# Performance work log

Measured on AMD Instinct MI355X. Metric: run time of the kernel, lower is better.

Reference implementation:

```python
import jax, jax.numpy as jnp
import numpy as np

B, L, INP, HID, NCLS = 512, 256, 300, 256, 5  # trees, leaves/tree, embed dim, hidden, classes


def setup_inputs() -> dict:
    key = jax.random.key(0)
    ks = jax.random.split(key, 7)
    s_in = 1.0 / np.sqrt(INP).astype(np.float32)
    s_h = 1.0 / np.sqrt(HID).astype(np.float32)
    # W_leaf order: [inp_gate, out_gate, upd_gate]
    # W_nl order:  [inp_ln, inp_rn, fo_l_l, fo_l_r, fo_r_l, fo_r_r, out_ln, out_rn, upd_ln, upd_rn]
    return {
        "embeddings": jax.random.normal(ks[0], (B, L, INP), jnp.float32),
        "W_leaf": jax.random.uniform(ks[1], (3, INP, HID), jnp.float32, -s_in, s_in),
        "b_leaf": jax.random.uniform(ks[2], (3, HID), jnp.float32, -s_in, s_in),
        "W_nl": jax.random.uniform(ks[3], (10, HID, HID), jnp.float32, -s_h, s_h),
        "b_nl": jax.random.uniform(ks[4], (10, HID), jnp.float32, -s_h, s_h),
        "W_out": jax.random.uniform(ks[5], (HID, NCLS), jnp.float32, -s_h, s_h),
        "b_out": jax.random.uniform(ks[6], (NCLS,), jnp.float32, -s_h, s_h),
    }


def reference(embeddings, W_leaf, b_leaf, W_nl, b_nl, W_out, b_out):
    sig, tanh = jax.nn.sigmoid, jnp.tanh
    # ---- leaf nodes (depth 0), batched over all B*L leaves ----
    pre = jnp.einsum('bli,gih->blgh', embeddings, W_leaf) + b_leaf  # [B,L,3,H]
    i_g = sig(pre[:, :, 0])
    o_g = sig(pre[:, :, 1])
    u_g = tanh(pre[:, :, 2])
    c = i_g * u_g                      # [B,L,H]
    h = o_g * sig(c)                   # note: leaf uses sigmoid(cell), as in torch code
    logits = [jnp.einsum('bnh,hc->bnc', h, W_out) + b_out]
    # ---- internal nodes, level-synchronous ----
    Wl = W_nl[0::2]                    # [5,H,H] acting on left hidden
    Wr = W_nl[1::2]                    # [5,H,H] acting on right hidden
    bb = b_nl[0::2] + b_nl[1::2]       # [5,H]
    n = L
    while n > 1:
        lc, rc = c[:, 0::2], c[:, 1::2]
        lh, rh = h[:, 0::2], h[:, 1::2]
        pre = (jnp.einsum('bnh,ghk->bngk', lh, Wl)
               + jnp.einsum('bnh,ghk->bngk', rh, Wr) + bb)  # [B,n/2,5,H]
        inp_g = sig(pre[:, :, 0])
        fol_g = sig(pre[:, :, 1])
        for_g = sig(pre[:, :, 2])
        out_g = sig(pre[:, :, 3])
        upd_g = tanh(pre[:, :, 4])
        c = inp_g * upd_g + fol_g * lc + for_g * rc
        h = out_g * tanh(c)
        logits.append(jnp.einsum('bnh,hc->bnc', h, W_out) + b_out)
        n //= 2
    # per-node class scores for all 2L-1 nodes (leaves first, root last)
    return jnp.concatenate(logits, axis=1)  # [B, 2L-1, NCLS]
```

## Files before the change

### kernel.cpp

```cpp
#include <hip/hip_runtime.h>
#include <hip/hip_bf16.h>


#define HID 256

typedef __attribute__((ext_vector_type(8))) short short8;
typedef __attribute__((ext_vector_type(4))) float f32x4;
typedef __attribute__((ext_vector_type(4))) unsigned short ushort4v;

__device__ __forceinline__ float rcpf(float x) { return __builtin_amdgcn_rcpf(x); }
__device__ __forceinline__ float sigf(float x) { return rcpf(1.0f + __expf(-x)); }
__device__ __forceinline__ float tanhf_(float x) { return 2.0f * rcpf(1.0f + __expf(-2.0f * x)) - 1.0f; }
__device__ __forceinline__ float bf2f(unsigned short u) {
    union { unsigned int i; float f; } v; v.i = ((unsigned int)u) << 16; return v.f;
}
__device__ __forceinline__ unsigned short f2bf(float f) {
    __hip_bfloat16 b = __float2bfloat16(f);
    return *(unsigned short*)&b;
}
__device__ __forceinline__ void gload_lds16(const void* g, void* l) {
    __builtin_amdgcn_global_load_lds(
        (const __attribute__((address_space(1))) unsigned int*)g,
        (__attribute__((address_space(3))) unsigned int*)l, 16, 0, 0);
}
template <int N> __device__ __forceinline__ void waitcnt_vm() {
    if constexpr (N == 0)       asm volatile("s_waitcnt vmcnt(0)" ::: "memory");
    else if constexpr (N == 9)  asm volatile("s_waitcnt vmcnt(9)" ::: "memory");
    else if constexpr (N == 10) asm volatile("s_waitcnt vmcnt(10)" ::: "memory");
    else                        asm volatile("s_waitcnt vmcnt(0)" ::: "memory");
}

template <int NG, int FG, int NCB, int K, bool LEAF>
__global__ __launch_bounds__(256, 2) void gemm_mid(
    const unsigned short* __restrict__ A,
    const unsigned short* __restrict__ BT,
    const float* __restrict__ bias,
    const float* __restrict__ cprev,
    float* __restrict__ cout,
    unsigned short* __restrict__ hout)
{
    constexpr int CW   = FG * 16;
    constexpr int GW   = 2 * CW;
    constexpr int BN   = NG * GW;
    constexpr int NK   = K / 64;
    constexpr int NBW  = BN / 32;
    constexpr int L    = 4 + NBW;
    constexpr int NF   = NG * FG;
    constexpr int ABUF = 128 * 128;
    constexpr int BBUF = BN * 128;
    constexpr int BUF  = ABUF + BBUF;

    __shared__ char smem[2 * BUF];

    const int t = threadIdx.x;
    const int lane = t & 63;
    const int w = t >> 6;
    const int wm = w >> 1, wn = w & 1;

    const int bid = blockIdx.x;
    const int xcd = bid & 7;
    const int slot = bid >> 3;
    const int cb = slot % NCB;
    const int row0 = ((slot / NCB) * 8 + xcd) * 128;

    const int l3 = lane >> 3;
    const unsigned int swsrc = (unsigned int)(((lane & 7) ^ l3) * 16);
    unsigned int a_src[4];
    unsigned int b_src[NBW];
#pragma unroll
    for (int q = 0; q < 4; ++q)
        a_src[q] = (unsigned int)(row0 + (w * 4 + q) * 8 + l3) * (K * 2) + swsrc;
#pragma unroll
    for (int q = 0; q < NBW; ++q)
        b_src[q] = (unsigned int)(cb * BN + (w * NBW + q) * 8 + l3) * (K * 2) + swsrc;

    const int swz0 = ((lane >> 4) ^ (lane & 7)) * 16;
    const int swz1 = (((lane >> 4) + 4) ^ (lane & 7)) * 16;
    const int aoff = (wm * 64 + (lane & 15)) * 128;
    const int boff = (wn * CW + (lane & 15)) * 128;

    f32x4 acc[4][NF] = {};

    auto STAGE = [&](int buf, int kt) {
        char* As = smem + buf * BUF;
        char* Bs = As + ABUF;
        const unsigned int k0b = (unsigned int)kt * 128;
#pragma unroll
        for (int q = 0; q < 4; ++q)
            gload_lds16((const char*)A + (size_t)(a_src[q] + k0b),
                        As + (w * 4 + q) * 1024);
#pragma unroll
        for (int q = 0; q < NBW; ++q)
            gload_lds16((const char*)BT + (size_t)(b_src[q] + k0b),
                        Bs + (w * NBW + q) * 1024);
    };

    STAGE(0, 0);
    STAGE(1, 1);

#pragma unroll
    for (int kt = 0; kt < NK; ++kt) {
        const int cur = kt & 1;
        if (kt + 1 < NK) waitcnt_vm<L>(); else waitcnt_vm<0>();
        __builtin_amdgcn_s_barrier();
        const char* As = smem + cur * BUF;
        const char* Bs = As + ABUF;
#pragma unroll
        for (int ks = 0; ks < 2; ++ks) {
            const int sw = ks ? swz1 : swz0;
            short8 a[4], b[NF];
#pragma unroll
            for (int mf = 0; mf < 4; ++mf)
                a[mf] = *(const short8*)(As + aoff + mf * 2048 + sw);
#pragma unroll
            for (int g = 0; g < NG; ++g)
#pragma unroll
                for (int fc = 0; fc < FG; ++fc)
                    b[g * FG + fc] = *(const short8*)(Bs + g * (GW * 128) +
                                                      fc * 2048 + boff + sw);
            __builtin_amdgcn_s_setprio(1);
#pragma unroll
            for (int f = 0; f < NF; ++f)
#pragma unroll
                for (int mf = 0; mf < 4; ++mf)
                    acc[mf][f] = __builtin_amdgcn_mfma_f32_16x16x32_bf16(
                        a[mf], b[f], acc[mf][f], 0, 0, 0);
            __builtin_amdgcn_s_setprio(0);
        }
        asm volatile("s_waitcnt lgkmcnt(0)" ::: "memory");
        __builtin_amdgcn_sched_barrier(0);
        __builtin_amdgcn_s_barrier();
        if (kt + 2 < NK) STAGE(cur, kt + 2);
    }

#pragma unroll
    for (int mf = 0; mf < 4; ++mf) {
#pragma unroll
        for (int j = 0; j < 4; ++j) {
            const int rl = wm * 64 + mf * 16 + ((lane >> 4) << 2) + j;
            const int r = row0 + rl;
#pragma unroll
            for (int fc = 0; fc < FG; ++fc) {
                const int cl = wn * CW + fc * 16 + (lane & 15);
                const int c = cb * GW + cl;
                float cv, hv;
                if constexpr (LEAF) {
                    float p0 = acc[mf][0 * FG + fc][j] + bias[c];
                    float p1 = acc[mf][1 * FG + fc][j] + bias[256 + c];
                    float p2 = acc[mf][2 * FG + fc][j] + bias[512 + c];
                    cv = sigf(p0) * tanhf_(p2);
                    hv = sigf(p1) * sigf(cv);
                } else {
                    float p0 = acc[mf][0 * FG + fc][j] + bias[c];
                    float p1 = acc[mf][1 * FG + fc][j] + bias[256 + c];
                    float p2 = acc[mf][2 * FG + fc][j] + bias[512 + c];
                    float p3 = acc[mf][3 * FG + fc][j] + bias[768 + c];
                    float p4 = acc[mf][4 * FG + fc][j] + bias[1024 + c];
                    float lc = cprev[(size_t)r * 512 + c];
                    float rc = cprev[(size_t)r * 512 + 256 + c];
                    cv = sigf(p0) * tanhf_(p4) + sigf(p1) * lc + sigf(p2) * rc;
                    hv = sigf(p3) * tanhf_(cv);
                }
                cout[(size_t)r * 256 + c] = cv;
                hout[(size_t)r * 256 + c] = f2bf(hv);
            }
        }
    }
}

template <int NG, int K>
__global__ __launch_bounds__(256, 3) void gemm_small(
    const unsigned short* __restrict__ A,
    const unsigned short* __restrict__ BT,
    const float* __restrict__ bias,
    const float* __restrict__ cprev,
    float* __restrict__ cout,
    unsigned short* __restrict__ hout)
{
    constexpr int CS  = 32;
    constexpr int BN  = NG * CS;
    constexpr int NK  = K / 64;
    constexpr int NBW = BN / 32;
    constexpr int ABUF = 128 * 128;

    __shared__ char smem[2 * ABUF + BN * 128];
    char* Bs = smem + 2 * ABUF;

    const int t = threadIdx.x;
    const int lane = t & 63;
    const int w = t >> 6;
    const int wm = w >> 1, wn = w & 1;
    const int cb = blockIdx.x;
    const int row0 = blockIdx.y * 128;

    const int l3 = lane >> 3;
    const unsigned int swsrc = (unsigned int)(((lane & 7) ^ l3) * 16);
    unsigned int a_src[4];
    unsigned int b_src[NBW];
#pragma unroll
    for (int q = 0; q < 4; ++q)
        a_src[q] = (unsigned int)(row0 + (w * 4 + q) * 8 + l3) * (K * 2) + swsrc;
#pragma unroll
    for (int q = 0; q < NBW; ++q)
        b_src[q] = (unsigned int)(cb * BN + (w * NBW + q) * 8 + l3) * (K * 2) + swsrc;

    const int swz0 = ((lane >> 4) ^ (lane & 7)) * 16;
    const int swz1 = (((lane >> 4) + 4) ^ (lane & 7)) * 16;
    const int aoff = (wm * 64 + (lane & 15)) * 128;
    const int boff = (wn * 16 + (lane & 15)) * 128;

    f32x4 acc[4][NG] = {};

    auto STAGE_A = [&](int buf, int kt) {
        char* As = smem + buf * ABUF;
        const unsigned int k0b = (unsigned int)kt * 128;
#pragma unroll
        for (int q = 0; q < 4; ++q)
            gload_lds16((const char*)A + (size_t)(a_src[q] + k0b),
                        As + (w * 4 + q) * 1024);
    };
    auto STAGE_B = [&](int kt) {
        const unsigned int k0b = (unsigned int)kt * 128;
#pragma unroll
        for (int q = 0; q < NBW; ++q)
            gload_lds16((const char*)BT + (size_t)(b_src[q] + k0b),
                        Bs + (w * NBW + q) * 1024);
    };

    STAGE_A(0, 0);
    STAGE_B(0);
    asm volatile("s_waitcnt vmcnt(0)" ::: "memory");
    __builtin_amdgcn_s_barrier();
    asm volatile("" ::: "memory");

#pragma unroll
    for (int kt = 0; kt < NK; ++kt) {
        const int cur = kt & 1;
        if (kt + 1 < NK) STAGE_A(cur ^ 1, kt + 1);
        const char* As = smem + cur * ABUF;
#pragma unroll
        for (int ks = 0; ks < 2; ++ks) {
            const int sw = ks ? swz1 : swz0;
            short8 a[4];
#pragma unroll
            for (int mf = 0; mf < 4; ++mf)
                a[mf] = *(const short8*)(As + aoff + mf * 2048 + sw);
#pragma unroll
            for (int g = 0; g < NG; ++g) {
                short8 b = *(const short8*)(Bs + g * (CS * 128) + boff + sw);
#pragma unroll
                for (int mf = 0; mf < 4; ++mf)
                    acc[mf][g] = __builtin_amdgcn_mfma_f32_16x16x32_bf16(
                        a[mf], b, acc[mf][g], 0, 0, 0);
            }
        }
        asm volatile("" ::: "memory");
        __builtin_amdgcn_s_barrier();
        asm volatile("" ::: "memory");
        if (kt + 1 < NK) {
            STAGE_B(kt + 1);
            asm volatile("s_waitcnt vmcnt(0)" ::: "memory");
        }
        __builtin_amdgcn_s_barrier();
        asm volatile("" ::: "memory");
    }

#pragma unroll
    for (int mf = 0; mf < 4; ++mf) {
#pragma unroll
        for (int j = 0; j < 4; ++j) {
            const int rl = wm * 64 + mf * 16 + ((lane >> 4) << 2) + j;
            const int r = row0 + rl;
            const int cl = wn * 16 + (lane & 15);
            const int c = cb * 32 + cl;
            float p0 = acc[mf][0][j] + bias[c];
            float p1 = acc[mf][1][j] + bias[256 + c];
            float p2 = acc[mf][2][j] + bias[512 + c];
            float p3 = acc[mf][3][j] + bias[768 + c];
            float p4 = acc[mf][4][j] + bias[1024 + c];
            float lc = cprev[(size_t)r * 512 + c];
            float rc = cprev[(size_t)r * 512 + 256 + c];
            float cv = sigf(p0) * tanhf_(p4) + sigf(p1) * lc + sigf(p2) * rc;
            float hv = sigf(p3) * tanhf_(cv);
            cout[(size_t)r * 256 + c] = cv;
            hout[(size_t)r * 256 + c] = f2bf(hv);
        }
    }
}

__global__ __launch_bounds__(256) void logits_all(
    const unsigned short* __restrict__ hA,
    const unsigned short* __restrict__ hRest,
    const float* __restrict__ W_out, const float* __restrict__ b_out,
    float* __restrict__ out)
{
    const int t = threadIdx.x;
    const int part = t & 15;
    const int rl = t >> 4;

    float wreg[80];
#pragma unroll
    for (int e = 0; e < 16; ++e)
#pragma unroll
        for (int cls = 0; cls < 5; ++cls)
            wreg[e * 5 + cls] = W_out[(part * 16 + e) * 5 + cls];
    const float b0 = b_out[0], b1 = b_out[1], b2 = b_out[2],
                b3 = b_out[3], b4 = b_out[4];

    for (int ch = blockIdx.x; ch < 16352; ch += gridDim.x) {
        const int R = ch * 16 + rl;
        const unsigned short* h = (R < 131072)
            ? hA + (size_t)R * HID
            : hRest + (size_t)(R - 131072) * HID;

        short8 h0 = *(const short8*)(h + part * 16);
        short8 h1 = *(const short8*)(h + part * 16 + 8);
        float a0 = 0.f, a1 = 0.f, a2 = 0.f, a3 = 0.f, a4 = 0.f;
#pragma unroll
        for (int e = 0; e < 8; ++e) {
            float f = bf2f((unsigned short)h0[e]);
            a0 = fmaf(f, wreg[e * 5 + 0], a0);
            a1 = fmaf(f, wreg[e * 5 + 1], a1);
            a2 = fmaf(f, wreg[e * 5 + 2], a2);
            a3 = fmaf(f, wreg[e * 5 + 3], a3);
            a4 = fmaf(f, wreg[e * 5 + 4], a4);
        }
#pragma unroll
        for (int e = 0; e < 8; ++e) {
            float f = bf2f((unsigned short)h1[e]);
            a0 = fmaf(f, wreg[(8 + e) * 5 + 0], a0);
            a1 = fmaf(f, wreg[(8 + e) * 5 + 1], a1);
            a2 = fmaf(f, wreg[(8 + e) * 5 + 2], a2);
            a3 = fmaf(f, wreg[(8 + e) * 5 + 3], a3);
            a4 = fmaf(f, wreg[(8 + e) * 5 + 4], a4);
        }
#pragma unroll
        for (int m = 8; m >= 1; m >>= 1) {
            a0 += __shfl_xor(a0, m);
            a1 += __shfl_xor(a1, m);
            a2 += __shfl_xor(a2, m);
            a3 += __shfl_xor(a3, m);
            a4 += __shfl_xor(a4, m);
        }
        if (part == 0) {
            unsigned int V = 262144u - (unsigned int)R;
            int lev = 17 - (31 - __clz(V - 1));
            int start = 262144 - (1 << (18 - lev));
            int local = R - start;
            int nb = 8 - lev;
            int b = local >> nb, j = local & ((1 << nb) - 1);
            int off = 512 - (1 << (9 - lev));
            size_t o = ((size_t)b * 511 + off + j) * 5;
            out[o + 0] = a0 + b0;
            out[o + 1] = a1 + b1;
            out[o + 2] = a2 + b2;
            out[o + 3] = a3 + b3;
            out[o + 4] = a4 + b4;
        }
    }
}

__global__ __launch_bounds__(256) void prep_weights(
    const float* __restrict__ W_leaf, const float* __restrict__ W_nl,
    const float* __restrict__ b_nl,
    unsigned short* __restrict__ BleafT,
    unsigned short* __restrict__ BlevT,
    float* __restrict__ bb)
{
    const int T1 = 768 * 320, T2 = 1280 * 512, T3 = 5 * 256;
    for (int idx = blockIdx.x * 256 + threadIdx.x; idx < T1 + T2 + T3;
         idx += gridDim.x * 256) {
        if (idx < T1) {
            int colp = idx / 320, k = idx % 320;
            int cbv = colp / 192, rem = colp % 192;
            int g = rem >> 6, cl = rem & 63;
            int c = cbv * 64 + cl;
            float v = (k < 300) ? W_leaf[((size_t)g * 300 + k) * 256 + c] : 0.0f;
            BleafT[(size_t)colp * 320 + k] = f2bf(v);
        } else if (idx < T1 + T2) {
            int i2 = idx - T1;
            int colp = i2 / 512, k = i2 % 512;
            int cb8 = colp / 160, rem = colp % 160;
            int g = rem >> 5, cl = rem & 31;
            int c = cb8 * 32 + cl;
            float v = W_nl[((size_t)(2 * g + (k >= 256)) * 256 + (k & 255)) * 256 + c];
            BlevT[(size_t)colp * 512 + k] = f2bf(v);
        } else {
            int i3 = idx - T1 - T2;
            bb[i3] = b_nl[(size_t)(i3 >> 8) * 512 + (i3 & 255)] +
                     b_nl[(size_t)(i3 >> 8) * 512 + 256 + (i3 & 255)];
        }
    }
}

__global__ __launch_bounds__(256) void emb_to_bf16(
    const float* __restrict__ emb, unsigned short* __restrict__ embB)
{
    const int total = 131072 * 80;
    for (int idx = blockIdx.x * 256 + threadIdx.x; idx < total;
         idx += gridDim.x * 256) {
        int r = idx / 80, q = idx % 80;
        ushort4v o;
        if (q < 75) {
            const float4 v = *(const float4*)(emb + (size_t)r * 300 + q * 4);
            o.x = f2bf(v.x); o.y = f2bf(v.y); o.z = f2bf(v.z); o.w = f2bf(v.w);
        } else {
            o.x = 0; o.y = 0; o.z = 0; o.w = 0;
        }
        *(ushort4v*)(embB + (size_t)r * 320 + q * 4) = o;
    }
}

extern "C" void kernel_launch(void* const* d_in, const int* in_sizes, int n_in,
                              void* d_out, int out_size, void* d_ws, size_t ws_size,
                              hipStream_t stream) {
    const float* emb    = (const float*)d_in[0];
    const float* W_leaf = (const float*)d_in[1];
    const float* b_leaf = (const float*)d_in[2];
    const float* W_nl   = (const float*)d_in[3];
    const float* b_nl   = (const float*)d_in[4];
    const float* W_out  = (const float*)d_in[5];
    const float* b_out  = (const float*)d_in[6];
    float* out = (float*)d_out;

    char* ws = (char*)d_ws;
    unsigned short* embB   = (unsigned short*)(ws);
    unsigned short* hRest  = (unsigned short*)(ws);
    unsigned short* BleafT = (unsigned short*)(ws + 83886080);
    unsigned short* BlevT  = (unsigned short*)(ws + 84377600);
    float*          bb     = (float*)(ws + 85688320);
    float*          cA     = (float*)(ws + 85693440);
    unsigned short* hA     = (unsigned short*)(ws + 219911168);
    float*          cB     = (float*)(ws + 287020032);

    prep_weights<<<1024, 256, 0, stream>>>(W_leaf, W_nl, b_nl, BleafT, BlevT, bb);
    emb_to_bf16<<<2048, 256, 0, stream>>>(emb, embB);

    gemm_mid<3, 2, 4, 320, true><<<4096, 256, 0, stream>>>(
        embB, BleafT, b_leaf, nullptr, cA, hA);

    const unsigned short* hp = hA;
    const float* cp = cA;
    size_t hoff = 0;
    for (int lev = 1; lev <= 8; ++lev) {
        int n = 1 << (8 - lev);
        int M = 512 * n;
        float* cd = (lev & 1) ? cB : cA;
        unsigned short* hd = hRest + hoff;
        if (M >= 16384) {
            gemm_mid<5, 1, 8, 512, false><<<(M / 128) * 8, 256, 0, stream>>>(
                hp, BlevT, bb, cp, cd, hd);
        } else {
            gemm_small<5, 512><<<dim3(8, M / 128), 256, 0, stream>>>(
                hp, BlevT, bb, cp, cd, hd);
        }
        cp = cd;
        hp = hd;
        hoff += (size_t)M * HID;
    }

    logits_all<<<2048, 256, 0, stream>>>(hA, hRest, W_out, b_out, out);
}
```

Measured before the change: 451.7 us.

## Replace gemm_mid with 8-wave 256-row tile kernel and interleaved prefetch phases

The 4-wave 128-row GEMM is replaced by an 8-wave, 512-thread kernel with 256-row by 64-column (times gate count) tiles. Per-wave B fragments are held in registers across the k-step, and the next stage's A and B loads are split into four phases interleaved with MFMA groups. The weights get a new column permutation to match the per-wave 16-column layout. The goal is more reuse of B per tile and better overlap of global-to-LDS traffic with matrix math. In exchange, each block uses more LDS and registers, occupancy drops to one block per CU, and there are extra barriers per k-step.

After: 470.1 us. +4.1%, slower.

```diff
diff --git a/kernel.cpp b/kernel.cpp
--- a/kernel.cpp
+++ b/kernel.cpp
@@ -23,15 +23,9 @@
         (const __attribute__((address_space(1))) unsigned int*)g,
         (__attribute__((address_space(3))) unsigned int*)l, 16, 0, 0);
 }
-template <int N> __device__ __forceinline__ void waitcnt_vm() {
-    if constexpr (N == 0)       asm volatile("s_waitcnt vmcnt(0)" ::: "memory");
-    else if constexpr (N == 9)  asm volatile("s_waitcnt vmcnt(9)" ::: "memory");
-    else if constexpr (N == 10) asm volatile("s_waitcnt vmcnt(10)" ::: "memory");
-    else                        asm volatile("s_waitcnt vmcnt(0)" ::: "memory");
-}
-
-template <int NG, int FG, int NCB, int K, bool LEAF>
-__global__ __launch_bounds__(256, 2) void gemm_mid(
+
+template <int NG, int K, bool LEAF>
+__global__ __launch_bounds__(512, 1) void gemm_big8(
     const unsigned short* __restrict__ A,
     const unsigned short* __restrict__ BT,
     const float* __restrict__ bias,
@@ -39,14 +33,11 @@
     float* __restrict__ cout,
     unsigned short* __restrict__ hout)
 {
-    constexpr int CW   = FG * 16;
-    constexpr int GW   = 2 * CW;
-    constexpr int BN   = NG * GW;
+    constexpr int BN   = NG * 64;
     constexpr int NK   = K / 64;
-    constexpr int NBW  = BN / 32;
-    constexpr int L    = 4 + NBW;
-    constexpr int NF   = NG * FG;
-    constexpr int ABUF = 128 * 128;
+    constexpr int NBW  = BN / 64;
+    constexpr int BP0  = (NBW + 1) / 2;
+    constexpr int ABUF = 256 * 128;
     constexpr int BBUF = BN * 128;
     constexpr int BUF  = ABUF + BBUF;
 
@@ -55,13 +46,13 @@
     const int t = threadIdx.x;
     const int lane = t & 63;
     const int w = t >> 6;
-    const int wm = w >> 1, wn = w & 1;
+    const int wm = w >> 2, wn = w & 3;
 
     const int bid = blockIdx.x;
     const int xcd = bid & 7;
     const int slot = bid >> 3;
-    const int cb = slot % NCB;
-    const int row0 = ((slot / NCB) * 8 + xcd) * 128;
+    const int cb = slot & 3;
+    const int row0 = ((slot >> 2) * 8 + xcd) * 256;
 
     const int l3 = lane >> 3;
     const unsigned int swsrc = (unsigned int)(((lane & 7) ^ l3) * 16);
@@ -76,94 +67,115 @@
 
     const int swz0 = ((lane >> 4) ^ (lane & 7)) * 16;
     const int swz1 = (((lane >> 4) + 4) ^ (lane & 7)) * 16;
-    const int aoff = (wm * 64 + (lane & 15)) * 128;
-    const int boff = (wn * CW + (lane & 15)) * 128;
-
-    f32x4 acc[4][NF] = {};
-
-    auto STAGE = [&](int buf, int kt) {
+    const int aoff = (wm * 128 + (lane & 15)) * 128;
+    const int boff = (wn * (NG * 16) + (lane & 15)) * 128;
+
+    f32x4 acc[8][NG] = {};
+    short8 breg[NG][2];
+
+    auto STAGE_A = [&](int buf, int kt, int half) {
         char* As = smem + buf * BUF;
-        char* Bs = As + ABUF;
         const unsigned int k0b = (unsigned int)kt * 128;
 #pragma unroll
-        for (int q = 0; q < 4; ++q)
+        for (int q = 2 * half; q < 2 * half + 2; ++q)
             gload_lds16((const char*)A + (size_t)(a_src[q] + k0b),
                         As + (w * 4 + q) * 1024);
-#pragma unroll
-        for (int q = 0; q < NBW; ++q)
+    };
+    auto STAGE_B = [&](int buf, int kt, int half) {
+        char* Bs = smem + buf * BUF + ABUF;
+        const unsigned int k0b = (unsigned int)kt * 128;
+        const int q0 = half ? BP0 : 0;
+        const int q1 = half ? NBW : BP0;
+#pragma unroll
+        for (int q = q0; q < q1; ++q)
             gload_lds16((const char*)BT + (size_t)(b_src[q] + k0b),
                         Bs + (w * NBW + q) * 1024);
     };
 
-    STAGE(0, 0);
-    STAGE(1, 1);
-
-#pragma unroll
+#define PHASE(MFB, STAGE_STMT, FINAL)                                         \
+    {                                                                          \
+        short8 a0k0 = *(const short8*)(As + aoff + (MFB) * 2048 + swz0);       \
+        short8 a0k1 = *(const short8*)(As + aoff + (MFB) * 2048 + swz1);       \
+        short8 a1k0 = *(const short8*)(As + aoff + (MFB + 1) * 2048 + swz0);   \
+        short8 a1k1 = *(const short8*)(As + aoff + (MFB + 1) * 2048 + swz1);   \
+        STAGE_STMT;                                                            \
+        asm volatile("" ::: "memory");                                         \
+        __builtin_amdgcn_s_barrier();                                          \
+        asm volatile("" ::: "memory");                                         \
+        __builtin_amdgcn_s_setprio(1);                                         \
+        _Pragma("unroll")                                                      \
+        for (int g = 0; g < NG; ++g) {                                         \
+            acc[MFB][g] = __builtin_amdgcn_mfma_f32_16x16x32_bf16(             \
+                a0k0, breg[g][0], acc[MFB][g], 0, 0, 0);                       \
+            acc[MFB + 1][g] = __builtin_amdgcn_mfma_f32_16x16x32_bf16(         \
+                a1k0, breg[g][0], acc[MFB + 1][g], 0, 0, 0);                   \
+            acc[MFB][g] = __builtin_amdgcn_mfma_f32_16x16x32_bf16(             \
+                a0k1, breg[g][1], acc[MFB][g], 0, 0, 0);                       \
+            acc[MFB + 1][g] = __builtin_amdgcn_mfma_f32_16x16x32_bf16(         \
+                a1k1, breg[g][1], acc[MFB + 1][g], 0, 0, 0);                   \
+        }                                                                      \
+        __builtin_amdgcn_s_setprio(0);                                         \
+        if (FINAL) {                                                           \
+            asm volatile("s_waitcnt lgkmcnt(0)" ::: "memory");                  \
+            __builtin_amdgcn_sched_barrier(0);                                  \
+        }                                                                      \
+        asm volatile("" ::: "memory");                                         \
+        __builtin_amdgcn_s_barrier();                                          \
+        asm volatile("" ::: "memory");                                         \
+    }
+
+    STAGE_A(0, 0, 0); STAGE_A(0, 0, 1);
+    STAGE_B(0, 0, 0); STAGE_B(0, 0, 1);
+
     for (int kt = 0; kt < NK; ++kt) {
         const int cur = kt & 1;
-        if (kt + 1 < NK) waitcnt_vm<L>(); else waitcnt_vm<0>();
-        __builtin_amdgcn_s_barrier();
         const char* As = smem + cur * BUF;
         const char* Bs = As + ABUF;
-#pragma unroll
-        for (int ks = 0; ks < 2; ++ks) {
-            const int sw = ks ? swz1 : swz0;
-            short8 a[4], b[NF];
-#pragma unroll
-            for (int mf = 0; mf < 4; ++mf)
-                a[mf] = *(const short8*)(As + aoff + mf * 2048 + sw);
-#pragma unroll
-            for (int g = 0; g < NG; ++g)
-#pragma unroll
-                for (int fc = 0; fc < FG; ++fc)
-                    b[g * FG + fc] = *(const short8*)(Bs + g * (GW * 128) +
-                                                      fc * 2048 + boff + sw);
-            __builtin_amdgcn_s_setprio(1);
-#pragma unroll
-            for (int f = 0; f < NF; ++f)
-#pragma unroll
-                for (int mf = 0; mf < 4; ++mf)
-                    acc[mf][f] = __builtin_amdgcn_mfma_f32_16x16x32_bf16(
-                        a[mf], b[f], acc[mf][f], 0, 0, 0);
-            __builtin_amdgcn_s_setprio(0);
-        }
-        asm volatile("s_waitcnt lgkmcnt(0)" ::: "memory");
-        __builtin_amdgcn_sched_barrier(0);
+        const bool pf = (kt + 1) < NK;
+
+        asm volatile("s_waitcnt vmcnt(0)" ::: "memory");
         __builtin_amdgcn_s_barrier();
-        if (kt + 2 < NK) STAGE(cur, kt + 2);
-    }
-
-#pragma unroll
-    for (int mf = 0; mf < 4; ++mf) {
+        asm volatile("" ::: "memory");
+
+#pragma unroll
+        for (int g = 0; g < NG; ++g) {
+            breg[g][0] = *(const short8*)(Bs + boff + g * 2048 + swz0);
+            breg[g][1] = *(const short8*)(Bs + boff + g * 2048 + swz1);
+        }
+        PHASE(0, if (pf) STAGE_A(cur ^ 1, kt + 1, 0), false)
+        PHASE(2, if (pf) STAGE_A(cur ^ 1, kt + 1, 1), false)
+        PHASE(4, if (pf) STAGE_B(cur ^ 1, kt + 1, 0), false)
+        PHASE(6, if (pf) STAGE_B(cur ^ 1, kt + 1, 1), true)
+    }
+#undef PHASE
+
+    const int cl = wn * 16 + (lane & 15);
+    const int c = cb * 64 + cl;
+#pragma unroll
+    for (int mf = 0; mf < 8; ++mf) {
 #pragma unroll
         for (int j = 0; j < 4; ++j) {
-            const int rl = wm * 64 + mf * 16 + ((lane >> 4) << 2) + j;
-            const int r = row0 + rl;
-#pragma unroll
-            for (int fc = 0; fc < FG; ++fc) {
-                const int cl = wn * CW + fc * 16 + (lane & 15);
-                const int c = cb * GW + cl;
-                float cv, hv;
-                if constexpr (LEAF) {
-                    float p0 = acc[mf][0 * FG + fc][j] + bias[c];
-                    float p1 = acc[mf][1 * FG + fc][j] + bias[256 + c];
-                    float p2 = acc[mf][2 * FG + fc][j] + bias[512 + c];
-                    cv = sigf(p0) * tanhf_(p2);
-                    hv = sigf(p1) * sigf(cv);
-                } else {
-                    float p0 = acc[mf][0 * FG + fc][j] + bias[c];
-                    float p1 = acc[mf][1 * FG + fc][j] + bias[256 + c];
-                    float p2 = acc[mf][2 * FG + fc][j] + bias[512 + c];
-                    float p3 = acc[mf][3 * FG + fc][j] + bias[768 + c];
-                    float p4 = acc[mf][4 * FG + fc][j] + bias[1024 + c];
-                    float lc = cprev[(size_t)r * 512 + c];
-                    float rc = cprev[(size_t)r * 512 + 256 + c];
-                    cv = sigf(p0) * tanhf_(p4) + sigf(p1) * lc + sigf(p2) * rc;
-                    hv = sigf(p3) * tanhf_(cv);
-                }
-                cout[(size_t)r * 256 + c] = cv;
-                hout[(size_t)r * 256 + c] = f2bf(hv);
+            const int r = row0 + wm * 128 + mf * 16 + ((lane >> 4) << 2) + j;
+            float cv, hv;
+            if constexpr (LEAF) {
+                float p0 = acc[mf][0][j] + bias[c];
+                float p1 = acc[mf][1][j] + bias[256 + c];
+                float p2 = acc[mf][2][j] + bias[512 + c];
+                cv = sigf(p0) * tanhf_(p2);
+                hv = sigf(p1) * sigf(cv);
+            } else {
+                float p0 = acc[mf][0][j] + bias[c];
+                float p1 = acc[mf][1][j] + bias[256 + c];
+                float p2 = acc[mf][2][j] + bias[512 + c];
+                float p3 = acc[mf][3][j] + bias[768 + c];
+                float p4 = acc[mf][4][j] + bias[1024 + c];
+                float lc = cprev[(size_t)r * 512 + c];
+                float rc = cprev[(size_t)r * 512 + 256 + c];
+                cv = sigf(p0) * tanhf_(p4) + sigf(p1) * lc + sigf(p2) * rc;
+                hv = sigf(p3) * tanhf_(cv);
             }
+            cout[(size_t)r * 256 + c] = cv;
+            hout[(size_t)r * 256 + c] = f2bf(hv);
         }
     }
 }
@@ -269,8 +281,7 @@
     for (int mf = 0; mf < 4; ++mf) {
 #pragma unroll
         for (int j = 0; j < 4; ++j) {
-            const int rl = wm * 64 + mf * 16 + ((lane >> 4) << 2) + j;
-            const int r = row0 + rl;
+            const int r = row0 + wm * 64 + mf * 16 + ((lane >> 4) << 2) + j;
             const int cl = wn * 16 + (lane & 15);
             const int c = cb * 32 + cl;
             float p0 = acc[mf][0][j] + bias[c];
@@ -364,29 +375,40 @@
     const float* __restrict__ W_leaf, const float* __restrict__ W_nl,
     const float* __restrict__ b_nl,
     unsigned short* __restrict__ BleafT,
-    unsigned short* __restrict__ BlevT,
+    unsigned short* __restrict__ BlevTn,
+    unsigned short* __restrict__ BlevTo,
     float* __restrict__ bb)
 {
-    const int T1 = 768 * 320, T2 = 1280 * 512, T3 = 5 * 256;
-    for (int idx = blockIdx.x * 256 + threadIdx.x; idx < T1 + T2 + T3;
+    const int T1 = 768 * 320, T2 = 1280 * 512, T3 = 1280 * 512, T4 = 5 * 256;
+    for (int idx = blockIdx.x * 256 + threadIdx.x; idx < T1 + T2 + T3 + T4;
          idx += gridDim.x * 256) {
         if (idx < T1) {
             int colp = idx / 320, k = idx % 320;
-            int cbv = colp / 192, rem = colp % 192;
-            int g = rem >> 6, cl = rem & 63;
-            int c = cbv * 64 + cl;
+            int cbv = colp / 192, r = colp % 192;
+            int wn = r / 48, r2 = r % 48;
+            int g = r2 >> 4, cl = r2 & 15;
+            int c = cbv * 64 + wn * 16 + cl;
             float v = (k < 300) ? W_leaf[((size_t)g * 300 + k) * 256 + c] : 0.0f;
             BleafT[(size_t)colp * 320 + k] = f2bf(v);
         } else if (idx < T1 + T2) {
             int i2 = idx - T1;
             int colp = i2 / 512, k = i2 % 512;
-            int cb8 = colp / 160, rem = colp % 160;
-            int g = rem >> 5, cl = rem & 31;
+            int cbv = colp / 320, r = colp % 320;
+            int wn = r / 80, r2 = r % 80;
+            int g = r2 >> 4, cl = r2 & 15;
+            int c = cbv * 64 + wn * 16 + cl;
+            float v = W_nl[((size_t)(2 * g + (k >= 256)) * 256 + (k & 255)) * 256 + c];
+            BlevTn[(size_t)colp * 512 + k] = f2bf(v);
+        } else if (idx < T1 + T2 + T3) {
+            int i2 = idx - T1 - T2;
+            int colp = i2 / 512, k = i2 % 512;
+            int cb8 = colp / 160, r = colp % 160;
+            int g = r >> 5, cl = r & 31;
             int c = cb8 * 32 + cl;
             float v = W_nl[((size_t)(2 * g + (k >= 256)) * 256 + (k & 255)) * 256 + c];
-            BlevT[(size_t)colp * 512 + k] = f2bf(v);
+            BlevTo[(size_t)colp * 512 + k] = f2bf(v);
         } else {
-            int i3 = idx - T1 - T2;
+            int i3 = idx - T1 - T2 - T3;
             bb[i3] = b_nl[(size_t)(i3 >> 8) * 512 + (i3 & 255)] +
                      b_nl[(size_t)(i3 >> 8) * 512 + 256 + (i3 & 255)];
         }
@@ -427,16 +449,18 @@
     unsigned short* embB   = (unsigned short*)(ws);
     unsigned short* hRest  = (unsigned short*)(ws);
     unsigned short* BleafT = (unsigned short*)(ws + 83886080);
-    unsigned short* BlevT  = (unsigned short*)(ws + 84377600);
-    float*          bb     = (float*)(ws + 85688320);
-    float*          cA     = (float*)(ws + 85693440);
-    unsigned short* hA     = (unsigned short*)(ws + 219911168);
-    float*          cB     = (float*)(ws + 287020032);
-
-    prep_weights<<<1024, 256, 0, stream>>>(W_leaf, W_nl, b_nl, BleafT, BlevT, bb);
+    unsigned short* BlevTn = (unsigned short*)(ws + 84377600);
+    unsigned short* BlevTo = (unsigned short*)(ws + 85688320);
+    float*          bb     = (float*)(ws + 86999040);
+    float*          cA     = (float*)(ws + 87004160);
+    unsigned short* hA     = (unsigned short*)(ws + 221221888);
+    float*          cB     = (float*)(ws + 288330752);
+
+    prep_weights<<<1024, 256, 0, stream>>>(W_leaf, W_nl, b_nl,
+                                           BleafT, BlevTn, BlevTo, bb);
     emb_to_bf16<<<2048, 256, 0, stream>>>(emb, embB);
 
-    gemm_mid<3, 2, 4, 320, true><<<4096, 256, 0, stream>>>(
+    gemm_big8<3, 320, true><<<2048, 512, 0, stream>>>(
         embB, BleafT, b_leaf, nullptr, cA, hA);
 
     const unsigned short* hp = hA;
@@ -448,11 +472,11 @@
         float* cd = (lev & 1) ? cB : cA;
         unsigned short* hd = hRest + hoff;
         if (M >= 16384) {
-            gemm_mid<5, 1, 8, 512, false><<<(M / 128) * 8, 256, 0, stream>>>(
-                hp, BlevT, bb, cp, cd, hd);
+            gemm_big8<5, 512, false><<<(M / 256) * 4, 512, 0, stream>>>(
+                hp, BlevTn, bb, cp, cd, hd);
         } else {
             gemm_small<5, 512><<<dim3(8, M / 128), 256, 0, stream>>>(
-                hp, BlevT, bb, cp, cd, hd);
+                hp, BlevTo, bb, cp, cd, hd);
         }
         cp = cd;
         hp = hd;
```
